# Performance work log

Measured on AMD Instinct MI355X. Metric: run time of the kernel, lower is better.

Reference implementation:

```python
import jax, jax.numpy as jnp
import numpy as np

B, L, N, C = 16, 12, 512, 3
SEQ = 12
FFT = SEQ // 2 + 1
EMB, ID_EMB, HID = 64, 64, 128
RC, DC, SC, EC = 32, 32, 256, 512
OUT, KS, BLOCKS, LAYERS = 12, 2, 4, 2
TID, DIW = 288, 7
K_SUB = 20
A_COEF = 0.5
NLAYERS = BLOCKS * LAYERS
DILATIONS = [1, 2] * BLOCKS
RECEPTIVE = 13  # 1 + blocks*(1+2) with kernel_size=2, layers=2


def setup_inputs() -> dict:
    key = jax.random.key(0)
    ks = jax.random.split(key, 20)
    r = jax.random.normal
    return {
        "history_data": jax.random.uniform(ks[0], (B, L, N, C), jnp.float32),
        "start_w": r(ks[1], (RC, 2)) * 0.1, "start_b": jnp.zeros((RC,)),
        "filt_w": r(ks[2], (NLAYERS, DC, RC, KS)) * 0.1, "filt_b": jnp.zeros((NLAYERS, DC)),
        "gate_w": r(ks[3], (NLAYERS, DC, RC, KS)) * 0.1, "gate_b": jnp.zeros((NLAYERS, DC)),
        "skip_w": r(ks[4], (NLAYERS, SC, DC)) * 0.1, "skip_b": jnp.zeros((NLAYERS, SC)),
        "gconv_w": r(ks[5], (NLAYERS, RC, 5 * DC)) * 0.1, "gconv_b": jnp.zeros((NLAYERS, RC)),
        "end1_w": r(ks[6], (EC, SC)) * 0.05, "end1_b": jnp.zeros((EC,)),
        "end2_w": r(ks[7], (OUT, EC)) * 0.05, "end2_b": jnp.zeros((OUT,)),
        "Ex1": r(ks[8], (FFT, EMB)) * 0.1,
        "node1": r(ks[9], (N, ID_EMB)) * 0.1,
        "Wd": r(ks[10], (N, EMB + ID_EMB + 2 * SEQ, HID)) * 0.05,
        "Wxabs": r(ks[11], (HID, HID)) * 0.05,
        "TiD_emb": r(ks[12], (TID, SEQ)) * 0.1,
        "DiW_emb": r(ks[13], (DIW, SEQ)) * 0.1,
        "nodevec1": r(ks[14], (N, EMB)) * 0.1,
        "nodevec2": r(ks[15], (EMB, N)) * 0.1,
    }


def conv1x1(x, w, b):
    # x: [B,C,N,L], w: [O,C] -> [B,O,N,L]
    return jnp.einsum('bcnl,oc->bonl', x, w) + b[None, :, None, None]


def tconv(x, w, b, d):
    # dilated (1,2) temporal conv; w: [O,C,2]
    lo = x[..., : x.shape[-1] - d]
    hi = x[..., d:]
    y = jnp.einsum('bcnl,oc->bonl', lo, w[..., 0]) + jnp.einsum('bcnl,oc->bonl', hi, w[..., 1])
    return y + b[None, :, None, None]


def nconv(x, A):
    if A.ndim == 2:
        return jnp.einsum('bcvl,vw->bcwl', x, A)
    return jnp.einsum('bcvl,bvw->bcwl', x, A)


def gcn(x, supports, w, b):
    out = [x]
    for A in supports:  # order = 2 hops per support
        x1 = nconv(x, A)
        out.append(x1)
        out.append(nconv(x1, A))
    return conv1x1(jnp.concatenate(out, axis=1), w, b)  # dropout is identity in eval


def _forward(history_data, start_w, start_b, filt_w, filt_b, gate_w, gate_b,
             skip_w, skip_b, gconv_w, gconv_b, end1_w, end1_b, end2_w, end2_b,
             Ex1, node1, Wd, Wxabs, TiD_emb, DiW_emb, nodevec1, nodevec2):
    inp = jnp.transpose(history_data, (0, 3, 2, 1))[:, 0:2]          # [B,2,N,L]
    x = jnp.pad(inp, ((0, 0), (0, 0), (0, 0), (RECEPTIVE - L, 0)))   # left-pad time
    x = conv1x1(x, start_w, start_b)                                  # [B,RC,N,13]

    # self-adaptive graph (Graph WaveNet)
    gwadp = jax.nn.softmax(jax.nn.relu(nodevec1 @ nodevec2), axis=1)  # [N,N]

    # dynamic frequency-domain graph
    xn1 = inp[:, 0, :, -SEQ:]                                         # [B,N,SEQ]
    freq = jnp.abs(jnp.fft.rfft(xn1, axis=-1))                        # [B,N,FFT]
    e = jnp.einsum('bnf,fk->bnk', freq, Ex1)                          # [B,N,EMB]
    e = jnp.concatenate([e, jnp.broadcast_to(node1, (B, N, ID_EMB))], axis=2)
    T_D = TiD_emb[(history_data[:, -1, :, 1] * TID).astype(jnp.int32)]  # [B,N,SEQ]
    D_W = DiW_emb[(history_data[:, -1, :, 2] * DIW).astype(jnp.int32)]  # [B,N,SEQ]
    e = jnp.concatenate([e, T_D, D_W], axis=2)                        # [B,N,EMB+ID+2*SEQ]
    adp = jnp.einsum('bne,nek->bnk', e, Wd)                           # per-node projection
    mu = adp.mean(axis=(1, 2), keepdims=True)
    var = adp.var(axis=(1, 2), keepdims=True)
    adp = (adp - mu) / jnp.sqrt(var + 1e-8)                           # LayerNorm [N,HID], no affine
    adj = jax.nn.relu(jnp.einsum('bnk,kj,bmj->bnm', adp, Wxabs, adp))  # [B,N,N]
    noise = jax.random.uniform(jax.random.key(42), adj.shape) * 0.01
    _, idx = jax.lax.top_k(adj + noise, K_SUB)                        # [B,N,K] row-wise topk
    mask = jnp.zeros_like(adj).at[
        jnp.arange(B)[:, None, None], jnp.arange(N)[None, :, None], idx].set(1.0)
    adj = jax.nn.softmax(adj * mask, axis=2)
    supports = [gwadp, A_COEF * adj]

    skip = None
    bn_scale = 1.0 / np.sqrt(1.0 + 1e-5)  # eval BatchNorm with default running stats
    for i in range(NLAYERS):
        residual = x
        f = jnp.tanh(tconv(residual, filt_w[i], filt_b[i], DILATIONS[i]))
        g = jax.nn.sigmoid(tconv(residual, gate_w[i], gate_b[i], DILATIONS[i]))
        x = f * g
        s = conv1x1(x, skip_w[i], skip_b[i])
        skip = s if skip is None else s + skip[..., -s.shape[-1]:]
        x = gcn(x, supports, gconv_w[i], gconv_b[i])
        x = x + residual[..., -x.shape[-1]:]
        x = x * bn_scale
    x = jax.nn.relu(skip)
    x = jax.nn.relu(conv1x1(x, end1_w, end1_b))
    return conv1x1(x, end2_w, end2_b)  # [B,OUT,N,1]


def reference(history_data, start_w, start_b, filt_w, filt_b, gate_w, gate_b,
              skip_w, skip_b, gconv_w, gconv_b, end1_w, end1_b, end2_w, end2_b,
              Ex1, node1, Wd, Wxabs, TiD_emb, DiW_emb, nodevec1, nodevec2):
    return _forward(history_data, start_w, start_b, filt_w, filt_b, gate_w, gate_b,
                    skip_w, skip_b, gconv_w, gconv_b, end1_w, end1_b, end2_w, end2_b,
                    Ex1, node1, Wd, Wxabs, TiD_emb, DiW_emb, nodevec1, nodevec2)
```

## Files before the change

### kernel.cpp

```cpp
#include <hip/hip_runtime.h>
#include <cstdint>
#include <math.h>

typedef unsigned short ushort_t;
typedef __bf16 bf16x8 __attribute__((ext_vector_type(8)));
typedef float f32x4 __attribute__((ext_vector_type(4)));

#define BNSCALE 0.9999950000374998f

__device__ __forceinline__ ushort_t f2b(float x){
  union { float f; uint32_t u; } v; v.f = x;
  uint32_t u = v.u;
  u = u + 0x7fffu + ((u >> 16) & 1u);
  return (ushort_t)(u >> 16);
}
__device__ __forceinline__ float b2f(ushort_t h){
  union { float f; uint32_t u; } v; v.u = ((uint32_t)h) << 16; return v.f;
}

__device__ __forceinline__ uint32_t rotl32(uint32_t x, int d){ return (x<<d)|(x>>(32-d)); }

__device__ __forceinline__ void threefry2x32(uint32_t& x0, uint32_t& x1){
  const uint32_t ks0=0u, ks1=42u, ks2=42u^0x1BD11BDAu;
  x0+=ks0; x1+=ks1;
  x0+=x1; x1=rotl32(x1,13); x1^=x0;
  x0+=x1; x1=rotl32(x1,15); x1^=x0;
  x0+=x1; x1=rotl32(x1,26); x1^=x0;
  x0+=x1; x1=rotl32(x1, 6); x1^=x0;
  x0+=ks1; x1+=ks2+1u;
  x0+=x1; x1=rotl32(x1,17); x1^=x0;
  x0+=x1; x1=rotl32(x1,29); x1^=x0;
  x0+=x1; x1=rotl32(x1,16); x1^=x0;
  x0+=x1; x1=rotl32(x1,24); x1^=x0;
  x0+=ks2; x1+=ks0+2u;
  x0+=x1; x1=rotl32(x1,13); x1^=x0;
  x0+=x1; x1=rotl32(x1,15); x1^=x0;
  x0+=x1; x1=rotl32(x1,26); x1^=x0;
  x0+=x1; x1=rotl32(x1, 6); x1^=x0;
  x0+=ks0; x1+=ks1+3u;
  x0+=x1; x1=rotl32(x1,17); x1^=x0;
  x0+=x1; x1=rotl32(x1,29); x1^=x0;
  x0+=x1; x1=rotl32(x1,16); x1^=x0;
  x0+=x1; x1=rotl32(x1,24); x1^=x0;
  x0+=ks1; x1+=ks2+4u;
  x0+=x1; x1=rotl32(x1,13); x1^=x0;
  x0+=x1; x1=rotl32(x1,15); x1^=x0;
  x0+=x1; x1=rotl32(x1,26); x1^=x0;
  x0+=x1; x1=rotl32(x1, 6); x1^=x0;
  x0+=ks2; x1+=ks0+5u;
}

__global__ void k_start(const float* __restrict__ hist, const float* __restrict__ sw,
                        const float* __restrict__ sb, float* __restrict__ x){
  int idx = blockIdx.x*256 + threadIdx.x;
  int n = idx & 511; int r = idx >> 9;
  int o = r & 31; int r2 = r >> 5;
  int t = r2 % 13; int b = r2 / 13;
  float acc = sb[o];
  if (t > 0){
    const float* h = hist + ((size_t)(b*12 + (t-1))*512 + n)*3;
    acc += h[0]*sw[o*2+0] + h[1]*sw[o*2+1];
  }
  x[(((size_t)(b*13 + t)*32 + o))*512 + n] = acc;
}

__global__ void k_gw_mm(const float* __restrict__ nv1, const float* __restrict__ nv2,
                        float* __restrict__ gw){
  int idx = blockIdx.x*256+threadIdx.x;
  int w = idx & 511, v = idx >> 9;
  float acc=0.f;
  #pragma unroll
  for (int k=0;k<64;k++) acc += nv1[v*64+k]*nv2[k*512+w];
  gw[idx]=acc;
}

__global__ void k_gw_sm(float* __restrict__ gw){
  int v = blockIdx.x; int tid=threadIdx.x;
  float a0 = fmaxf(gw[v*512+tid],0.f), a1=fmaxf(gw[v*512+256+tid],0.f);
  __shared__ float red[256];
  red[tid]=fmaxf(a0,a1); __syncthreads();
  for(int s=128;s>0;s>>=1){ if(tid<s) red[tid]=fmaxf(red[tid],red[tid+s]); __syncthreads(); }
  float m = red[0]; __syncthreads();
  float e0=expf(a0-m), e1=expf(a1-m);
  red[tid]=e0+e1; __syncthreads();
  for(int s=128;s>0;s>>=1){ if(tid<s) red[tid]+=red[tid+s]; __syncthreads(); }
  float inv = 1.0f/red[0];
  gw[v*512+tid]=e0*inv; gw[v*512+256+tid]=e1*inv;
}

__global__ void k_embed(const float* __restrict__ hist, const float* __restrict__ Ex1,
                        const float* __restrict__ node1, const float* __restrict__ TiD,
                        const float* __restrict__ DiW, float* __restrict__ e){
  const float c12[12] = {1.f, 0.8660254037844387f, 0.5f, 0.f, -0.5f, -0.8660254037844387f,
                         -1.f, -0.8660254037844387f, -0.5f, 0.f, 0.5f, 0.8660254037844387f};
  const float s12[12] = {0.f, -0.5f, -0.8660254037844387f, -1.f, -0.8660254037844387f, -0.5f,
                         0.f, 0.5f, 0.8660254037844387f, 1.f, 0.8660254037844387f, 0.5f};
  int row = blockIdx.x; int b = row >> 9; int n = row & 511;
  int tid = threadIdx.x;
  __shared__ float fr[7];
  if (tid < 7){
    float re=0.f, im=0.f;
    for (int l=0;l<12;l++){
      float v = hist[((size_t)(b*12+l)*512+n)*3];
      int idx = (tid*l) % 12;
      re += v*c12[idx]; im += v*s12[idx];
    }
    fr[tid]=sqrtf(re*re+im*im);
  }
  __syncthreads();
  float* er = e + (size_t)row*152;
  float acc=0.f;
  #pragma unroll
  for (int f=0;f<7;f++) acc += fr[f]*Ex1[f*64+tid];
  er[tid]=acc;
  er[64+tid]=node1[n*64+tid];
  if (tid<12){
    int it = (int)(hist[((size_t)(b*12+11)*512+n)*3+1]*288.0f);
    int id = (int)(hist[((size_t)(b*12+11)*512+n)*3+2]*7.0f);
    er[128+tid]=TiD[it*12+tid];
    er[140+tid]=DiW[id*12+tid];
  }
}

__global__ void k_adp(const float* __restrict__ e, const float* __restrict__ Wd,
                      float* __restrict__ adp){
  int n = blockIdx.x; int tid = threadIdx.x;
  __shared__ float es[16][152];
  for (int idx = tid; idx < 16*152; idx += 128){
    int r = idx / 152, q = idx - r*152;
    es[r][q] = e[((size_t)(r*512+n))*152 + q];
  }
  __syncthreads();
  const float* w = Wd + (size_t)n*152*128;
  float acc[16];
  #pragma unroll
  for (int r=0;r<16;r++) acc[r]=0.f;
  for (int q = 0; q < 152; q++){
    float wv = w[q*128 + tid];
    #pragma unroll
    for (int r = 0; r < 16; r++) acc[r] += es[r][q]*wv;
  }
  #pragma unroll
  for (int r=0;r<16;r++) adp[((size_t)(r*512+n))*128 + tid] = acc[r];
}

__global__ void k_lnp1(const float* __restrict__ adp, float* __restrict__ part){
  int blk = blockIdx.x; int tid = threadIdx.x;
  const float* p = adp + (size_t)(blk>>4)*65536 + (size_t)(blk&15)*4096;
  float s=0.f, s2=0.f;
  for (int i=tid;i<4096;i+=256){ float v=p[i]; s+=v; s2+=v*v; }
  __shared__ float rs[256], rs2[256];
  rs[tid]=s; rs2[tid]=s2; __syncthreads();
  for(int k=128;k>0;k>>=1){ if(tid<k){rs[tid]+=rs[tid+k]; rs2[tid]+=rs2[tid+k];} __syncthreads(); }
  if(tid==0){ part[blk*2]=rs[0]; part[blk*2+1]=rs2[0]; }
}

__global__ void k_lnp2(const float* __restrict__ part, float* __restrict__ stats){
  int tid = threadIdx.x;
  int b = tid >> 4, c = tid & 15;
  float s = part[tid*2], s2 = part[tid*2+1];
  #pragma unroll
  for (int off=8; off>=1; off>>=1){ s += __shfl_down(s,off); s2 += __shfl_down(s2,off); }
  if (c==0){
    float mu = s/65536.f; float var = s2/65536.f - mu*mu;
    stats[b*2]=mu; stats[b*2+1]=rsqrtf(var+1e-8f);
  }
}

__global__ void k_xw(const float* __restrict__ adp, const float* __restrict__ Wx,
                     const float* __restrict__ stats, float* __restrict__ t){
  int row=blockIdx.x; int tid=threadIdx.x; int b=row>>9;
  __shared__ float as[128];
  as[tid]=(adp[(size_t)row*128+tid]-stats[2*b])*stats[2*b+1];
  __syncthreads();
  float acc=0.f;
  #pragma unroll 8
  for(int k=0;k<128;k++) acc += as[k]*Wx[k*128+tid];
  t[(size_t)row*128+tid]=acc;
}

__global__ __launch_bounds__(256) void k_adjmm(const float* __restrict__ T,
                        const float* __restrict__ P, const float* __restrict__ stats,
                        float* __restrict__ adj){
  int b = blockIdx.z;
  int n0 = blockIdx.y*32, m0 = blockIdx.x*64;
  const float* Tb = T + (size_t)b*512*128;
  const float* Pb = P + (size_t)b*512*128;
  float mu = stats[2*b], isig = stats[2*b+1];
  __shared__ float Ts[32][33];
  __shared__ float Ps[64][33];
  int tid=threadIdx.x; int tx=tid&15, ty=tid>>4;
  float acc[2][4]={};
  for(int k0=0;k0<128;k0+=32){
    for(int q=0;q<4;q++){ int idx=tid+q*256; int r=idx>>5, kk=idx&31; Ts[r][kk]=Tb[(size_t)(n0+r)*128+k0+kk]; }
    for(int q=0;q<8;q++){ int idx=tid+q*256; int r=idx>>5, kk=idx&31; Ps[r][kk]=(Pb[(size_t)(m0+r)*128+k0+kk]-mu)*isig; }
    __syncthreads();
    #pragma unroll
    for(int kk=0;kk<32;kk++){
      float t0=Ts[ty][kk], t1=Ts[ty+16][kk];
      float p0=Ps[tx*4+0][kk], p1=Ps[tx*4+1][kk], p2=Ps[tx*4+2][kk], p3=Ps[tx*4+3][kk];
      acc[0][0]+=t0*p0; acc[0][1]+=t0*p1; acc[0][2]+=t0*p2; acc[0][3]+=t0*p3;
      acc[1][0]+=t1*p0; acc[1][1]+=t1*p1; acc[1][2]+=t1*p2; acc[1][3]+=t1*p3;
    }
    __syncthreads();
  }
  for(int i2=0;i2<2;i2++){
    int n=n0+ty+16*i2;
    float4 o4=make_float4(fmaxf(acc[i2][0],0.f),fmaxf(acc[i2][1],0.f),
                          fmaxf(acc[i2][2],0.f),fmaxf(acc[i2][3],0.f));
    *(float4*)&adj[((size_t)b*512+n)*512+m0+tx*4]=o4;
  }
}

__global__ void k_topk(float* __restrict__ adj){
  const int row = blockIdx.x;
  const int tid = threadIdx.x;
  const uint32_t halfn = 2097152u;
  float a[8], v[8];
  const bool lowhalf = row < 4096;
  #pragma unroll
  for(int k=0;k<8;k++){
    int m = k*64+tid;
    uint32_t i = (uint32_t)row*512u + (uint32_t)m;
    uint32_t c0 = lowhalf ? i : i - halfn;
    uint32_t x0=c0, x1=c0+halfn;
    threefry2x32(x0,x1);
    uint32_t bits = lowhalf ? x0 : x1;
    float u = __uint_as_float((bits>>9)|0x3f800000u)-1.0f;
    a[k]=adj[(size_t)row*512+m];
    v[k]=a[k]+0.01f*u;
  }
  unsigned selmask=0u;
  for(int it=0; it<20; it++){
    float best=-1e30f; int bi=0x7fffffff;
    #pragma unroll
    for(int k=0;k<8;k++){
      if(!((selmask>>k)&1u)){
        int m=k*64+tid;
        if(v[k]>best || (v[k]==best && m<bi)){best=v[k]; bi=m;}
      }
    }
    #pragma unroll
    for(int off=32; off>=1; off>>=1){
      float ov=__shfl_xor(best,off); int oi=__shfl_xor(bi,off);
      if(ov>best || (ov==best && oi<bi)){best=ov; bi=oi;}
    }
    if((bi&63)==tid) selmask |= 1u<<(bi>>6);
  }
  float M=0.f;
  #pragma unroll
  for(int k=0;k<8;k++) if((selmask>>k)&1u) M=fmaxf(M,a[k]);
  #pragma unroll
  for(int off=32;off>=1;off>>=1) M=fmaxf(M,__shfl_xor(M,off));
  float S=0.f;
  #pragma unroll
  for(int k=0;k<8;k++) S += expf((((selmask>>k)&1u)? a[k]:0.f) - M);
  #pragma unroll
  for(int off=32;off>=1;off>>=1) S += __shfl_xor(S,off);
  float inv = 0.5f/S;
  #pragma unroll
  for(int k=0;k<8;k++){
    int m=k*64+tid;
    adj[(size_t)row*512+m] = expf((((selmask>>k)&1u)? a[k]:0.f)-M)*inv;
  }
}

__global__ void k_split(const float* __restrict__ src, ushort_t* __restrict__ hi,
                        ushort_t* __restrict__ lo, int count){
  int i = blockIdx.x*256+threadIdx.x;
  if (i < count){
    float v = src[i];
    ushort_t h = f2b(v);
    hi[i] = h;
    lo[i] = f2b(v - b2f(h));
  }
}

__global__ void k_splitT(const float* __restrict__ src, long sBS,
                         ushort_t* __restrict__ hi, long hBS, int hRS,
                         ushort_t* __restrict__ lo, long lBS, int lRS){
  int b = blockIdx.z;
  int c0 = blockIdx.x*32, r0 = blockIdx.y*32;
  __shared__ float tile[32][33];
  int tx = threadIdx.x & 31, ty = threadIdx.x >> 5;
  for (int q = 0; q < 4; q++)
    tile[ty+q*8][tx] = src[b*sBS + (size_t)(r0+ty+q*8)*512 + c0+tx];
  __syncthreads();
  for (int q = 0; q < 4; q++){
    int cc = c0+ty+q*8, rr = r0+tx;
    float v = tile[tx][ty+q*8];
    ushort_t h = f2b(v);
    hi[b*hBS + (size_t)cc*hRS + rr] = h;
    lo[b*lBS + (size_t)cc*lRS + rr] = f2b(v - b2f(h));
  }
}

__global__ __launch_bounds__(256,2) void k_pow(
    const ushort_t* __restrict__ Ah, const ushort_t* __restrict__ Al, long aBS,
    const ushort_t* __restrict__ Bh, const ushort_t* __restrict__ Bl, long bBS,
    ushort_t* __restrict__ Ch, ushort_t* __restrict__ Cl, long cBS){
  __shared__ __align__(16) ushort_t At[5120];
  __shared__ __align__(16) ushort_t Bt[5120];
  const int b = blockIdx.z;
  const int r0 = blockIdx.x*64, n0 = blockIdx.y*64;
  const int tid = threadIdx.x;
  const int w = tid >> 6, l = tid & 63, lr = l & 15, kg = l >> 4;
  const int wr = w & 1, wc = w >> 1;
  const int ra = tid >> 2, ca = (tid & 3)*8;
  const ushort_t* Ahp = Ah + (long)b*aBS + (long)(r0+ra)*512 + ca;
  const ushort_t* Alp = Al + (long)b*aBS + (long)(r0+ra)*512 + ca;
  const ushort_t* Bhp = Bh + (long)b*bBS + (long)(n0+ra)*512 + ca;
  const ushort_t* Blp = Bl + (long)b*bBS + (long)(n0+ra)*512 + ca;
  f32x4 acc[2][2];
  #pragma unroll
  for (int ms=0; ms<2; ms++)
    #pragma unroll
    for (int ns=0; ns<2; ns++) acc[ms][ns] = (f32x4){0.f,0.f,0.f,0.f};
  uint4 pA0,pA1,pB0,pB1;
  #define LDP(K0) { \
    pA0 = *(const uint4*)(Ahp + (K0)); pA1 = *(const uint4*)(Alp + (K0)); \
    pB0 = *(const uint4*)(Bhp + (K0)); pB1 = *(const uint4*)(Blp + (K0)); }
  LDP(0);
  for (int k0 = 0; k0 < 512; k0 += 32){
    __syncthreads();
    *(uint4*)&At[ra*40 + ca]        = pA0;
    *(uint4*)&At[2560 + ra*40 + ca] = pA1;
    *(uint4*)&Bt[ra*40 + ca]        = pB0;
    *(uint4*)&Bt[2560 + ra*40 + ca] = pB1;
    __syncthreads();
    if (k0 + 32 < 512) LDP(k0 + 32);
    bf16x8 ahv[2], alv[2], bhv[2], blv[2];
    #pragma unroll
    for (int ms=0; ms<2; ms++){
      int ar = wr*32 + ms*16 + lr;
      ahv[ms] = *(const bf16x8*)&At[ar*40 + kg*8];
      alv[ms] = *(const bf16x8*)&At[2560 + ar*40 + kg*8];
    }
    #pragma unroll
    for (int ns=0; ns<2; ns++){
      int br = wc*32 + ns*16 + lr;
      bhv[ns] = *(const bf16x8*)&Bt[br*40 + kg*8];
      blv[ns] = *(const bf16x8*)&Bt[2560 + br*40 + kg*8];
    }
    #pragma unroll
    for (int ms=0; ms<2; ms++)
      #pragma unroll
      for (int ns=0; ns<2; ns++){
        acc[ms][ns] = __builtin_amdgcn_mfma_f32_16x16x32_bf16(ahv[ms], bhv[ns], acc[ms][ns], 0, 0, 0);
        acc[ms][ns] = __builtin_amdgcn_mfma_f32_16x16x32_bf16(alv[ms], bhv[ns], acc[ms][ns], 0, 0, 0);
        acc[ms][ns] = __builtin_amdgcn_mfma_f32_16x16x32_bf16(ahv[ms], blv[ns], acc[ms][ns], 0, 0, 0);
      }
  }
  #undef LDP
  #pragma unroll
  for (int ms=0; ms<2; ms++)
    #pragma unroll
    for (int rg=0; rg<4; rg++){
      int r = r0 + wr*32 + ms*16 + kg*4 + rg;
      #pragma unroll
      for (int ns=0; ns<2; ns++){
        int n = n0 + wc*32 + ns*16 + lr;
        float v = acc[ms][ns][rg];
        long ofs = (long)b*cBS + (long)r*512 + n;
        ushort_t hv = f2b(v);
        Ch[ofs] = hv;
        Cl[ofs] = f2b(v - b2f(hv));
      }
    }
}

__global__ __launch_bounds__(256,1) void k_gemms(
    const ushort_t* __restrict__ Afh, const ushort_t* __restrict__ Afl,
    const ushort_t* __restrict__ S0h, const ushort_t* __restrict__ S0l,
    const ushort_t* __restrict__ S1h, const ushort_t* __restrict__ S1l,
    const ushort_t* __restrict__ S2h, const ushort_t* __restrict__ S2l,
    const ushort_t* __restrict__ S3h, const ushort_t* __restrict__ S3l,
    const float* __restrict__ gcw, float* __restrict__ xnew,
    int Mt, int M, int lo){
  __shared__ __align__(16) char smem[51200];
  ushort_t* At = (ushort_t*)smem;
  ushort_t* Bt = (ushort_t*)(smem + 10240);
  float* m32 = (float*)smem;
  float* Wgs = (float*)(smem + 16896);
  const int total = gridDim.x;
  const int chunk = total >> 3;
  const int lid = blockIdx.x;
  const int swz = (lid & 7)*chunk + (lid >> 3);
  const int x = swz % Mt;
  const int rest = swz / Mt;
  const int y = rest & 7;
  const int b = rest >> 3;
  const int n0 = y*64, r0 = x*64;
  const int tid = threadIdx.x;
  const int w = tid >> 6, l = tid & 63, lr = l & 15, kg = l >> 4;
  const int ra = tid >> 2, ca = (tid & 3)*8;
  int arow = r0 + ra; if (arow >= M) arow = M - 1;
  const ushort_t* Ahp = Afh + (long)b*M*512 + (long)arow*512 + ca;
  const ushort_t* Alp = Afl + (long)b*M*512 + (long)arow*512 + ca;
  const int zz = w, rb = l;
  const ushort_t* Bz; const ushort_t* Bzl;
  if (zz == 0){ Bz = S0h; Bzl = S0l; }
  else if (zz == 1){ Bz = S1h; Bzl = S1l; }
  else if (zz == 2){ Bz = S2h + (long)b*262144; Bzl = S2l + (long)b*262144; }
  else { Bz = S3h + (long)b*262144; Bzl = S3l + (long)b*262144; }
  const ushort_t* Bhp = Bz + (long)(n0 + rb)*512;
  const ushort_t* Blp = Bzl + (long)(n0 + rb)*512;

  f32x4 acc[4][4];
  #pragma unroll
  for (int ms=0; ms<4; ms++)
    #pragma unroll
    for (int ns=0; ns<4; ns++) acc[ms][ns] = (f32x4){0.f,0.f,0.f,0.f};

  uint4 pA0,pA1,pB0,pB1,pB2,pB3,pB4,pB5,pB6,pB7;
  #define LDG(K0) { \
    pA0 = *(const uint4*)(Ahp + (K0)); pA1 = *(const uint4*)(Alp + (K0)); \
    pB0 = *(const uint4*)(Bhp + (K0));      pB1 = *(const uint4*)(Bhp + (K0) + 8); \
    pB2 = *(const uint4*)(Bhp + (K0) + 16); pB3 = *(const uint4*)(Bhp + (K0) + 24); \
    pB4 = *(const uint4*)(Blp + (K0));      pB5 = *(const uint4*)(Blp + (K0) + 8); \
    pB6 = *(const uint4*)(Blp + (K0) + 16); pB7 = *(const uint4*)(Blp + (K0) + 24); }
  LDG(0);
  for (int k0 = 0; k0 < 512; k0 += 32){
    __syncthreads();
    *(uint4*)&At[ra*40 + ca]        = pA0;
    *(uint4*)&At[2560 + ra*40 + ca] = pA1;
    {
      ushort_t* bb = Bt + zz*5120 + rb*40;
      *(uint4*)&bb[0]  = pB0; *(uint4*)&bb[8]  = pB1;
      *(uint4*)&bb[16] = pB2; *(uint4*)&bb[24] = pB3;
      ushort_t* bl2 = bb + 2560;
      *(uint4*)&bl2[0]  = pB4; *(uint4*)&bl2[8]  = pB5;
      *(uint4*)&bl2[16] = pB6; *(uint4*)&bl2[24] = pB7;
    }
    __syncthreads();
    if (k0 + 32 < 512) LDG(k0 + 32);
    bf16x8 ahv[4], alv[4];
    #pragma unroll
    for (int ms=0; ms<4; ms++){
      int ar = ms*16 + lr;
      ahv[ms] = *(const bf16x8*)&At[ar*40 + kg*8];
      alv[ms] = *(const bf16x8*)&At[2560 + ar*40 + kg*8];
    }
    #pragma unroll
    for (int ns=0; ns<4; ns++){
      int br = ns*16 + lr;
      bf16x8 bh = *(const bf16x8*)&Bt[w*5120 + br*40 + kg*8];
      bf16x8 bl = *(const bf16x8*)&Bt[w*5120 + 2560 + br*40 + kg*8];
      #pragma unroll
      for (int ms=0; ms<4; ms++){
        acc[ms][ns] = __builtin_amdgcn_mfma_f32_16x16x32_bf16(ahv[ms], bh, acc[ms][ns], 0, 0, 0);
        acc[ms][ns] = __builtin_amdgcn_mfma_f32_16x16x32_bf16(alv[ms], bh, acc[ms][ns], 0, 0, 0);
        acc[ms][ns] = __builtin_amdgcn_mfma_f32_16x16x32_bf16(ahv[ms], bl, acc[ms][ns], 0, 0, 0);
      }
    }
  }
  #undef LDG
  __syncthreads();
  for (int idx = tid; idx < 4096; idx += 256){
    int z = idx >> 10, rem = idx & 1023;
    int c2 = rem >> 5, c = rem & 31;
    Wgs[idx] = gcw[c*160 + (z+1)*32 + c2];
  }
  const int g = tid >> 6, j = tid & 63;
  float outv[32];
  #pragma unroll
  for (int c=0; c<32; c++) outv[c] = 0.f;
  #pragma unroll
  for (int z=0; z<4; z++){
    __syncthreads();
    if (w == z){
      #pragma unroll
      for (int ms=0; ms<4; ms++)
        #pragma unroll
        for (int ns=0; ns<4; ns++)
          #pragma unroll
          for (int rg=0; rg<4; rg++)
            m32[(ms*16 + kg*4 + rg)*66 + ns*16 + lr] = acc[ms][ns][rg];
    }
    __syncthreads();
    if (tid < 128){
      const float* wzT = Wgs + z*1024;
      for (int c2=0; c2<32; c2++){
        float yv = m32[(g*32 + c2)*66 + j];
        const float* wrow = wzT + c2*32;
        #pragma unroll
        for (int c=0; c<32; c++) outv[c] += wrow[c]*yv;
      }
    }
  }
  if (tid < 128 && r0 + g*32 < M){
    int t = (r0 >> 5) + g;
    long ob = ((long)(b*lo + t)*32)*512 + n0 + j;
    #pragma unroll
    for (int c=0; c<32; c++){
      long ofs = ob + (long)c*512;
      xnew[ofs] += outv[c]*BNSCALE;
    }
  }
}

__global__ void k_mix1(const float* __restrict__ x,
    const float* __restrict__ fw, const float* __restrict__ fb,
    const float* __restrict__ gwv, const float* __restrict__ gb,
    const float* __restrict__ gcw, const float* __restrict__ gcb,
    ushort_t* __restrict__ fgh, ushort_t* __restrict__ fgl,
    float* __restrict__ fgL, float* __restrict__ xnew,
    int d, int li, int lo){
  __shared__ float FWs[2048], GWs[2048], W0s[1024];
  __shared__ float fbs[32], gbs[32], gcbs[32];
  int tid = threadIdx.x;
  int t = blockIdx.y, b = blockIdx.z;
  int n = blockIdx.x*256 + tid;
  for (int idx = tid; idx < 2048; idx += 256){ FWs[idx] = fw[idx]; GWs[idx] = gwv[idx]; }
  for (int idx = tid; idx < 1024; idx += 256) W0s[idx] = gcw[(idx>>5)*160 + (idx&31)];
  if (tid < 32){ fbs[tid]=fb[tid]; gbs[tid]=gb[tid]; gcbs[tid]=gcb[tid]; }
  __syncthreads();
  float xv[32], xv2[32], fgv[32];
  const float* xb  = x + ((size_t)(b*li + t)*32)*512 + n;
  const float* xb2 = x + ((size_t)(b*li + t + d)*32)*512 + n;
  #pragma unroll
  for (int c=0;c<32;c++){ xv[c] = xb[(size_t)c*512]; xv2[c] = xb2[(size_t)c*512]; }
  #pragma unroll
  for (int o=0;o<32;o++){
    float f = fbs[o], g = gbs[o];
    #pragma unroll
    for (int c=0;c<32;c++){
      float2 wf = *(const float2*)&FWs[(o*32+c)*2];
      float2 wg = *(const float2*)&GWs[(o*32+c)*2];
      f += xv[c]*wf.x + xv2[c]*wf.y;
      g += xv[c]*wg.x + xv2[c]*wg.y;
    }
    f = fminf(f, 15.f);
    float e2 = __expf(2.f*f);
    float th = (e2 - 1.f)/(e2 + 1.f);
    float sg = 1.f/(1.f + __expf(-g));
    fgv[o] = th*sg;
  }
  size_t rbase = ((size_t)(b*lo + t)*32)*512 + n;
  #pragma unroll
  for (int o=0;o<32;o++){
    float bs = gcbs[o] + xv2[o];
    #pragma unroll
    for (int c=0;c<32;c++) bs += W0s[o*32+c]*fgv[c];
    xnew[rbase + (size_t)o*512] = bs*BNSCALE;
    ushort_t h = f2b(fgv[o]);
    fgh[rbase + (size_t)o*512] = h;
    fgl[rbase + (size_t)o*512] = f2b(fgv[o] - b2f(h));
  }
  if (t == lo-1){
    #pragma unroll
    for (int o=0;o<32;o++) fgL[((size_t)b*32+o)*512 + n] = fgv[o];
  }
}

__global__ void k_skipacc(const float* __restrict__ fgL, const float* __restrict__ sw,
                          const float* __restrict__ sb, float* __restrict__ skip, int init){
  int b = blockIdx.z; int sq = blockIdx.y; int n0 = blockIdx.x*64;
  int tid = threadIdx.x; int col = tid & 63; int q = tid >> 6;
  __shared__ float fgls[32][65];
  for (int idx = tid; idx < 2048; idx += 256){
    int c = idx >> 6, j = idx & 63;
    fgls[c][j] = fgL[((size_t)b*32+c)*512 + n0 + j];
  }
  __syncthreads();
  int s0 = sq*64 + q*16;
  for (int s = s0; s < s0+16; s++){
    float acc = sb[s];
    #pragma unroll
    for (int c = 0; c < 32; c++) acc += sw[s*32+c]*fgls[c][col];
    size_t o = ((size_t)b*256+s)*512 + n0+col;
    skip[o] = init ? acc : skip[o] + acc;
  }
}

__global__ __launch_bounds__(256) void k_end1t(const float* __restrict__ skip,
                        const float* __restrict__ w, const float* __restrict__ bias,
                        float* __restrict__ h){
  int b = blockIdx.z; int e0 = blockIdx.y*32; int n0 = blockIdx.x*64;
  __shared__ float Ws_[32][33];
  __shared__ float Ss_[32][64];
  int tid = threadIdx.x, tx = tid&15, ty = tid>>4;
  float acc[2][4] = {};
  for (int k0 = 0; k0 < 256; k0 += 32){
    for (int q2 = 0; q2 < 4; q2++){ int idx = tid + q2*256; int r = idx>>5, kk = idx&31;
      Ws_[r][kk] = w[(size_t)(e0+r)*256 + k0+kk]; }
    for (int q2 = 0; q2 < 8; q2++){ int idx = tid + q2*256; int r = idx>>6, ww = idx&63;
      Ss_[r][ww] = fmaxf(skip[(size_t)b*131072 + (size_t)(k0+r)*512 + n0+ww], 0.f); }
    __syncthreads();
    #pragma unroll
    for (int kk = 0; kk < 32; kk++){
      float t0 = Ws_[ty][kk], t1 = Ws_[ty+16][kk];
      float4 b4 = *(float4*)&Ss_[kk][tx*4];
      acc[0][0]+=t0*b4.x; acc[0][1]+=t0*b4.y; acc[0][2]+=t0*b4.z; acc[0][3]+=t0*b4.w;
      acc[1][0]+=t1*b4.x; acc[1][1]+=t1*b4.y; acc[1][2]+=t1*b4.z; acc[1][3]+=t1*b4.w;
    }
    __syncthreads();
  }
  for (int i2 = 0; i2 < 2; i2++){
    int e = e0 + ty + 16*i2;
    float bb = bias[e];
    float4 o4 = make_float4(fmaxf(acc[i2][0]+bb,0.f), fmaxf(acc[i2][1]+bb,0.f),
                            fmaxf(acc[i2][2]+bb,0.f), fmaxf(acc[i2][3]+bb,0.f));
    *(float4*)&h[(size_t)b*262144 + (size_t)e*512 + n0 + tx*4] = o4;
  }
}

__global__ void k_end2(const float* __restrict__ h, const float* __restrict__ w,
                       const float* __restrict__ bias, float* __restrict__ out){
  int n = blockIdx.x*256+threadIdx.x; int o=blockIdx.y; int b=blockIdx.z;
  float acc=bias[o];
  const float* hb=h + (size_t)b*262144 + n;
  #pragma unroll 8
  for (int e=0;e<512;e++) acc += w[o*512+e]*hb[(size_t)e*512];
  out[((size_t)b*12+o)*512+n]=acc;
}

extern "C" void kernel_launch(void* const* d_in, const int* in_sizes, int n_in,
                              void* d_out, int out_size, void* d_ws, size_t ws_size,
                              hipStream_t stream) {
  (void)in_sizes; (void)n_in; (void)out_size;
  const float* hist   =(const float*)d_in[0];
  const float* start_w=(const float*)d_in[1];
  const float* start_b=(const float*)d_in[2];
  const float* filt_w =(const float*)d_in[3];
  const float* filt_b =(const float*)d_in[4];
  const float* gate_w =(const float*)d_in[5];
  const float* gate_b =(const float*)d_in[6];
  const float* skip_w =(const float*)d_in[7];
  const float* skip_b =(const float*)d_in[8];
  const float* gconv_w=(const float*)d_in[9];
  const float* gconv_b=(const float*)d_in[10];
  const float* end1_w =(const float*)d_in[11];
  const float* end1_b =(const float*)d_in[12];
  const float* end2_w =(const float*)d_in[13];
  const float* end2_b =(const float*)d_in[14];
  const float* Ex1    =(const float*)d_in[15];
  const float* node1  =(const float*)d_in[16];
  const float* Wd     =(const float*)d_in[17];
  const float* Wxabs  =(const float*)d_in[18];
  const float* TiD    =(const float*)d_in[19];
  const float* DiW    =(const float*)d_in[20];
  const float* nv1    =(const float*)d_in[21];
  const float* nv2    =(const float*)d_in[22];

  char* ws = (char*)d_ws;
  const size_t needed = 83902464;
  if (ws_size < needed) return;

  ushort_t* PtA_hi  = (ushort_t*)(ws + 0);
  ushort_t* PtA_lo  = (ushort_t*)(ws + 524288);
  ushort_t* PtA2_hi = (ushort_t*)(ws + 1048576);
  ushort_t* PtA2_lo = (ushort_t*)(ws + 1572864);
  ushort_t* PtB_hi  = (ushort_t*)(ws + 2097152);
  ushort_t* PtB_lo  = (ushort_t*)(ws + 10485760);
  ushort_t* PtB2_hi = (ushort_t*)(ws + 18874368);
  ushort_t* PtB2_lo = (ushort_t*)(ws + 27262976);
  float*    stats   = (float*)(ws + 35651584);
  float*    part    = (float*)(ws + 35651712);
  float*    skip    = (float*)(ws + 35667968);
  float*    fgL     = (float*)(ws + 44056576);
  ushort_t* fgh     = (ushort_t*)(ws + 45105152);
  ushort_t* fgl     = (ushort_t*)(ws + 51396608);
  float*    xA      = (float*)(ws + 57688064);
  float*    xB      = (float*)(ws + 71319552);
  float*    gwb     = (float*)(ws + 44056576);
  ushort_t* gws_hi  = (ushort_t*)(ws + 45105152);
  ushort_t* gws_lo  = (ushort_t*)(ws + 45629440);
  float*    ebuf    = (float*)(ws + 46153728);
  ushort_t* adjh    = (ushort_t*)(ws + 46153728);
  float*    adp     = (float*)(ws + 51134464);
  float*    xw      = (float*)(ws + 55328768);
  float*    adjb    = (float*)(ws + 59523072);
  ushort_t* adjl    = (ushort_t*)(ws + 76300288);
  float*    hbuf    = (float*)(ws + 45105152);

  k_embed<<<dim3(8192),dim3(64),0,stream>>>(hist,Ex1,node1,TiD,DiW,ebuf);
  k_adp<<<dim3(512),dim3(128),0,stream>>>(ebuf,Wd,adp);
  k_gw_mm<<<dim3(1024),dim3(256),0,stream>>>(nv1,nv2,gwb);
  k_gw_sm<<<dim3(512),dim3(256),0,stream>>>(gwb);
  k_split<<<dim3(1024),dim3(256),0,stream>>>(gwb, gws_hi, gws_lo, 262144);
  k_splitT<<<dim3(16,16,1),dim3(256),0,stream>>>(gwb, 0, PtA_hi, 0, 512, PtA_lo, 0, 512);
  k_pow<<<dim3(8,8,1),dim3(256),0,stream>>>(
      PtA_hi, PtA_lo, 0, gws_hi, gws_lo, 0, PtA2_hi, PtA2_lo, 0);
  k_lnp1<<<dim3(256),dim3(256),0,stream>>>(adp,part);
  k_lnp2<<<dim3(1),dim3(256),0,stream>>>(part,stats);
  k_xw<<<dim3(8192),dim3(128),0,stream>>>(adp,Wxabs,stats,xw);
  k_adjmm<<<dim3(8,16,16),dim3(256),0,stream>>>(xw,adp,stats,adjb);
  k_topk<<<dim3(8192),dim3(64),0,stream>>>(adjb);
  k_splitT<<<dim3(16,16,16),dim3(256),0,stream>>>(adjb, 262144, PtB_hi, 262144, 512,
                                                  PtB_lo, 262144, 512);
  k_split<<<dim3(16384),dim3(256),0,stream>>>(adjb, adjh, adjl, 4194304);
  k_pow<<<dim3(8,8,16),dim3(256),0,stream>>>(
      PtB_hi, PtB_lo, 262144, adjh, adjl, 262144, PtB2_hi, PtB2_lo, 262144);

  k_start<<<dim3(13312),dim3(256),0,stream>>>(hist,start_w,start_b,xA);

  const int lin[8]={13,12,10,9,7,6,4,3};
  const int dil[8]={1,2,1,2,1,2,1,2};
  float* xcur=xA; float* alt=xB;
  for (int i=0;i<8;i++){
    int d=dil[i], li=lin[i], lo=li-d;
    const float* fwp=filt_w+(size_t)i*2048; const float* fbp=filt_b+i*32;
    const float* gwp=gate_w+(size_t)i*2048; const float* gbp=gate_b+i*32;
    const float* swp=skip_w+(size_t)i*8192; const float* sbp=skip_b+i*256;
    const float* gcwp=gconv_w+(size_t)i*5120; const float* gcbp=gconv_b+i*32;
    int M = 32*lo, Mt = (M+63)/64;

    k_mix1<<<dim3(2,lo,16),dim3(256),0,stream>>>(xcur,fwp,fbp,gwp,gbp,gcwp,gcbp,
        fgh,fgl,fgL,alt,d,li,lo);
    k_skipacc<<<dim3(8,4,16),dim3(256),0,stream>>>(fgL,swp,sbp,skip,(i==0)?1:0);

    if (i < 7){
      k_gemms<<<dim3(Mt*8*16),dim3(256),0,stream>>>(
          fgh, fgl,
          PtA_hi, PtA_lo, PtA2_hi, PtA2_lo, PtB_hi, PtB_lo, PtB2_hi, PtB2_lo,
          gcwp, alt, Mt, M, lo);
    }
    float* tmp=xcur; xcur=alt; alt=tmp;
  }

  k_end1t<<<dim3(8,16,16),dim3(256),0,stream>>>(skip,end1_w,end1_b,hbuf);
  k_end2<<<dim3(2,12,16),dim3(256),0,stream>>>(hbuf,end2_w,end2_b,(float*)d_out);
}
```

Measured before the change: 1.260 ms.

## Double-buffer A tile in LDS and halve barriers in k_gemms main loop

The A tile in the k_gemms main loop now alternates between two LDS buffers. The next tile's global-to-LDS stores happen after the MFMAs, so each k-step needs one __syncthreads instead of two. B fragments are loaded into registers before the MFMA block, since each wave's B region is private and can be overwritten after reading. s_setprio raises wave priority around the MFMA block. LDS use grows from 50 KB to 60 KB, and the epilogue's m32/Wgs scratch now overlaps the A double buffer, which relies on the final in-loop barrier.

After: 1.259 ms. Within noise of the previous version (-0.1%).

```diff
diff --git a/kernel.cpp b/kernel.cpp
--- a/kernel.cpp
+++ b/kernel.cpp
@@ -377,9 +377,9 @@
     const ushort_t* __restrict__ S3h, const ushort_t* __restrict__ S3l,
     const float* __restrict__ gcw, float* __restrict__ xnew,
     int Mt, int M, int lo){
-  __shared__ __align__(16) char smem[51200];
+  __shared__ __align__(16) char smem[61440];
   ushort_t* At = (ushort_t*)smem;
-  ushort_t* Bt = (ushort_t*)(smem + 10240);
+  ushort_t* Bt = (ushort_t*)(smem + 20480);
   float* m32 = (float*)smem;
   float* Wgs = (float*)(smem + 16896);
   const int total = gridDim.x;
@@ -397,14 +397,14 @@
   int arow = r0 + ra; if (arow >= M) arow = M - 1;
   const ushort_t* Ahp = Afh + (long)b*M*512 + (long)arow*512 + ca;
   const ushort_t* Alp = Afl + (long)b*M*512 + (long)arow*512 + ca;
-  const int zz = w, rb = l;
   const ushort_t* Bz; const ushort_t* Bzl;
-  if (zz == 0){ Bz = S0h; Bzl = S0l; }
-  else if (zz == 1){ Bz = S1h; Bzl = S1l; }
-  else if (zz == 2){ Bz = S2h + (long)b*262144; Bzl = S2l + (long)b*262144; }
+  if (w == 0){ Bz = S0h; Bzl = S0l; }
+  else if (w == 1){ Bz = S1h; Bzl = S1l; }
+  else if (w == 2){ Bz = S2h + (long)b*262144; Bzl = S2l + (long)b*262144; }
   else { Bz = S3h + (long)b*262144; Bzl = S3l + (long)b*262144; }
-  const ushort_t* Bhp = Bz + (long)(n0 + rb)*512;
-  const ushort_t* Blp = Bzl + (long)(n0 + rb)*512;
+  const ushort_t* Bhp = Bz + (long)(n0 + l)*512;
+  const ushort_t* Blp = Bzl + (long)(n0 + l)*512;
+  ushort_t* myB = Bt + w*5120;
 
   f32x4 acc[4][4];
   #pragma unroll
@@ -419,43 +419,55 @@
     pB2 = *(const uint4*)(Bhp + (K0) + 16); pB3 = *(const uint4*)(Bhp + (K0) + 24); \
     pB4 = *(const uint4*)(Blp + (K0));      pB5 = *(const uint4*)(Blp + (K0) + 8); \
     pB6 = *(const uint4*)(Blp + (K0) + 16); pB7 = *(const uint4*)(Blp + (K0) + 24); }
+  #define WRA(P) { \
+    *(uint4*)&At[(P)*5120 + ra*40 + ca]        = pA0; \
+    *(uint4*)&At[(P)*5120 + 2560 + ra*40 + ca] = pA1; }
+  #define WRB() { \
+    ushort_t* bb = myB + l*40; \
+    *(uint4*)&bb[0]  = pB0; *(uint4*)&bb[8]  = pB1; \
+    *(uint4*)&bb[16] = pB2; *(uint4*)&bb[24] = pB3; \
+    ushort_t* bl2 = bb + 2560; \
+    *(uint4*)&bl2[0]  = pB4; *(uint4*)&bl2[8]  = pB5; \
+    *(uint4*)&bl2[16] = pB6; *(uint4*)&bl2[24] = pB7; }
+
   LDG(0);
+  WRA(0); WRB();
+  __syncthreads();
   for (int k0 = 0; k0 < 512; k0 += 32){
-    __syncthreads();
-    *(uint4*)&At[ra*40 + ca]        = pA0;
-    *(uint4*)&At[2560 + ra*40 + ca] = pA1;
-    {
-      ushort_t* bb = Bt + zz*5120 + rb*40;
-      *(uint4*)&bb[0]  = pB0; *(uint4*)&bb[8]  = pB1;
-      *(uint4*)&bb[16] = pB2; *(uint4*)&bb[24] = pB3;
-      ushort_t* bl2 = bb + 2560;
-      *(uint4*)&bl2[0]  = pB4; *(uint4*)&bl2[8]  = pB5;
-      *(uint4*)&bl2[16] = pB6; *(uint4*)&bl2[24] = pB7;
-    }
-    __syncthreads();
-    if (k0 + 32 < 512) LDG(k0 + 32);
+    const int p = (k0 >> 5) & 1;
+    const bool hasnext = (k0 + 32 < 512);
+    if (hasnext) LDG(k0 + 32);
     bf16x8 ahv[4], alv[4];
     #pragma unroll
     for (int ms=0; ms<4; ms++){
       int ar = ms*16 + lr;
-      ahv[ms] = *(const bf16x8*)&At[ar*40 + kg*8];
-      alv[ms] = *(const bf16x8*)&At[2560 + ar*40 + kg*8];
-    }
+      ahv[ms] = *(const bf16x8*)&At[p*5120 + ar*40 + kg*8];
+      alv[ms] = *(const bf16x8*)&At[p*5120 + 2560 + ar*40 + kg*8];
+    }
+    bf16x8 bhv[4], blv[4];
     #pragma unroll
     for (int ns=0; ns<4; ns++){
       int br = ns*16 + lr;
-      bf16x8 bh = *(const bf16x8*)&Bt[w*5120 + br*40 + kg*8];
-      bf16x8 bl = *(const bf16x8*)&Bt[w*5120 + 2560 + br*40 + kg*8];
+      bhv[ns] = *(const bf16x8*)&myB[br*40 + kg*8];
+      blv[ns] = *(const bf16x8*)&myB[2560 + br*40 + kg*8];
+    }
+    __builtin_amdgcn_s_setprio(1);
+    #pragma unroll
+    for (int ns=0; ns<4; ns++){
       #pragma unroll
       for (int ms=0; ms<4; ms++){
-        acc[ms][ns] = __builtin_amdgcn_mfma_f32_16x16x32_bf16(ahv[ms], bh, acc[ms][ns], 0, 0, 0);
-        acc[ms][ns] = __builtin_amdgcn_mfma_f32_16x16x32_bf16(alv[ms], bh, acc[ms][ns], 0, 0, 0);
-        acc[ms][ns] = __builtin_amdgcn_mfma_f32_16x16x32_bf16(ahv[ms], bl, acc[ms][ns], 0, 0, 0);
+        acc[ms][ns] = __builtin_amdgcn_mfma_f32_16x16x32_bf16(ahv[ms], bhv[ns], acc[ms][ns], 0, 0, 0);
+        acc[ms][ns] = __builtin_amdgcn_mfma_f32_16x16x32_bf16(alv[ms], bhv[ns], acc[ms][ns], 0, 0, 0);
+        acc[ms][ns] = __builtin_amdgcn_mfma_f32_16x16x32_bf16(ahv[ms], blv[ns], acc[ms][ns], 0, 0, 0);
       }
     }
+    __builtin_amdgcn_s_setprio(0);
+    if (hasnext){ WRA(p^1); WRB(); }
+    __syncthreads();
   }
   #undef LDG
-  __syncthreads();
+  #undef WRA
+  #undef WRB
   for (int idx = tid; idx < 4096; idx += 256){
     int z = idx >> 10, rem = idx & 1023;
     int c2 = rem >> 5, c = rem & 31;
```
